# Kernel optimization log

Measured on AMD Instinct MI355X. Metric: run time of the kernel, lower is better.

Reference implementation:

```python
import jax, jax.numpy as jnp
import numpy as np
import math

B, N, M = 128, 32, 64           # batch, num_agents, num_other
OBS, ACT = 128, 16              # obs_input_dim, num_actions
D_QK = 128                      # obs_output_dim (== obs_output_dim_other)
D_AV = 64                       # obs_act_output_dim (== other)
F_IN = OBS + ACT                # obs_act_input_dim = 144


def _xavier(key, shape):
    fan_in, fan_out = shape[0], shape[1]
    limit = math.sqrt(6.0 / (fan_in + fan_out))
    return jax.random.uniform(key, shape, jnp.float32, -limit, limit)


def setup_inputs() -> dict:
    key = jax.random.key(0)
    ks = jax.random.split(key, 13)
    return {
        "states": jax.random.normal(ks[0], (B, N, OBS), jnp.float32),
        "policies": jax.random.uniform(ks[1], (B, N, ACT), jnp.float32),
        "actions": jax.random.uniform(ks[2], (B, N, ACT), jnp.float32),
        "states_other": jax.random.normal(ks[3], (B, M, OBS), jnp.float32),
        "actions_other": jax.random.uniform(ks[4], (B, M, ACT), jnp.float32),
        # weights stored as [in, out] (x @ W == nn.Linear without bias)
        "W_key": _xavier(ks[5], (OBS, D_QK)),
        "W_query": _xavier(ks[6], (OBS, D_QK)),
        "W_av": _xavier(ks[7], (F_IN, D_AV)),
        "W_key_other": _xavier(ks[8], (OBS, D_QK)),
        "W_query_other": _xavier(ks[9], (OBS, D_QK)),
        "W_av_other": _xavier(ks[10], (F_IN, D_AV)),
        "W_f1": _xavier(ks[11], (2 * D_AV, 64)),
        "W_f2": _xavier(ks[12], (64, 1)),
    }


def reference(states, policies, actions, states_other, actions_other,
              W_key, W_query, W_av, W_key_other, W_query_other,
              W_av_other, W_f1, W_f2):
    b, n, _ = states.shape
    obs_actions = jnp.concatenate([states, actions], axis=-1)   # [B,N,F_IN]
    obs_policy = jnp.concatenate([states, policies], axis=-1)   # [B,N,F_IN]

    key_obs = states @ W_key                                    # [B,N,D_QK]
    query_obs = states @ W_query                                # [B,N,D_QK]
    d_k = W_key.shape[1]
    weight = jax.nn.softmax(
        jnp.einsum('bid,bjd->bij', query_obs, key_obs) / math.sqrt(d_k), axis=-1)
    ret_weight = weight

    # place_policies is identity on (j,k): oap[b,j,k] = obs_policy[b,k] if j==k else obs_actions[b,k]
    eye = jnp.eye(n, dtype=states.dtype)[None, :, :, None]       # [1,N,N,1]
    oap = eye * obs_policy[:, None, :, :] + (1.0 - eye) * obs_actions[:, None, :, :]
    attention_values = jnp.tanh(oap @ W_av)                      # [B,N,N,D_AV] (j,k)

    # repeat-mul-sum == weighted reduction over k: wav[b,i,j,d] = sum_k w[b,i,k] av[b,j,k,d]
    wav = jnp.einsum('bik,bjkd->bijd', weight, attention_values)  # [B,N,N,D_AV]

    obs_actions_other = jnp.concatenate([states_other, actions_other], axis=-1)
    keys_other = states_other @ W_key_other                      # [B,M,D_QK]
    query_agent = states @ W_query_other                         # [B,N,D_QK]
    av_other = jnp.tanh(obs_actions_other @ W_av_other)          # [B,M,D_AV]
    d_k_o = W_key_other.shape[1]
    weight_other = jax.nn.softmax(
        jnp.einsum('bid,bmd->bim', query_agent, keys_other) / math.sqrt(d_k_o), axis=-1)
    wav_other = jnp.einsum('bim,bmd->bid', weight_other, av_other)  # [B,N,D_AV]

    # broadcast the per-agent other-branch features across the j axis for the concat
    wav_other_b = jnp.broadcast_to(wav_other[:, :, None, :], wav.shape[:-1] + (wav_other.shape[-1],))
    node_features = jnp.concatenate([wav, wav_other_b], axis=-1)  # [B,N,N,2*D_AV]

    h = jax.nn.leaky_relu(node_features @ W_f1, negative_slope=0.01)
    value = h @ W_f2                                              # [B,N,N,1]
    return value, ret_weight, weight_other
```

## Files before the change

kernel.cpp:

```cpp
#include <hip/hip_runtime.h>
#include <math.h>

#define WS_WQK   0
#define WS_WQKO  16384
#define WS_AVA   32768
#define WS_AVO   294912
#define WS_DPROJ 819200

#define INV_SQRT_DK 0.08838834764831845f

__device__ __forceinline__ float dot4(float4 a, float4 b) {
  return a.x*b.x + a.y*b.y + a.z*b.z + a.w*b.w;
}
__device__ __forceinline__ void fma4(float4& a, const float4 w, const float s) {
  a.x += w.x*s; a.y += w.y*s; a.z += w.z*s; a.w += w.w*s;
}

__global__ __launch_bounds__(256) void k1_pre(
    const float* __restrict__ g_states, const float* __restrict__ g_pol,
    const float* __restrict__ g_act, const float* __restrict__ g_so,
    const float* __restrict__ g_ao,
    const float* __restrict__ Wq, const float* __restrict__ Wk,
    const float* __restrict__ Wqo, const float* __restrict__ Wko,
    const float* __restrict__ W_av, const float* __restrict__ W_avo,
    const float* __restrict__ W_f1, float* __restrict__ ws)
{
  __shared__ __align__(16) float pool[8448];
  const int t = threadIdx.x;
  int blk = blockIdx.x;

  if (blk < 32) {
    const float* A; const float* Bm; float* O;
    if (blk < 16) { A = Wq;  Bm = Wk;  O = ws + WS_WQK; }
    else          { A = Wqo; Bm = Wko; O = ws + WS_WQKO; blk -= 16; }
    const int tr = (blk >> 2) << 5;
    const int tc = (blk & 3) << 5;
    float* sA = pool;
    float* sB = pool + 4224;
    const float4* a4 = (const float4*)(A + tr * 128);
    const float4* b4 = (const float4*)(Bm + tc * 128);
    #pragma unroll
    for (int u = 0; u < 4; ++u) {
      int f = t + u * 256;
      int r = f >> 5, c4 = f & 31;
      *(float4*)(sA + r*132 + c4*4) = a4[f];
      *(float4*)(sB + r*132 + c4*4) = b4[f];
    }
    __syncthreads();
    const int e = t & 31, cl0 = t >> 5;
    float acc[4] = {0,0,0,0};
    #pragma unroll 4
    for (int d4 = 0; d4 < 32; ++d4) {
      float4 bv = *(const float4*)(sB + e*132 + d4*4);
      #pragma unroll
      for (int rr = 0; rr < 4; ++rr) {
        float4 av = *(const float4*)(sA + (cl0 + rr*8)*132 + d4*4);
        acc[rr] += dot4(av, bv);
      }
    }
    #pragma unroll
    for (int rr = 0; rr < 4; ++rr)
      O[(tr + cl0 + rr*8)*128 + tc + e] = acc[rr];
    return;
  }
  blk -= 32;

  if (blk < 128) {
    const int b = blk;
    float* s_pre = pool;
    float* s_dl  = pool + 4224;
    {
      const int wv_  = t >> 6;
      const int ap   = wv_ & 1;
      const int rh   = wv_ >> 1;
      const int lane = t & 63;
      const float* gs = g_states + b*4096 + rh*16*128;
      const float* gt = (ap ? g_pol : g_act) + b*512 + rh*16*16;
      float acc[16];
      #pragma unroll
      for (int r = 0; r < 16; ++r) acc[r] = 0.f;
      #pragma unroll 4
      for (int c4 = 0; c4 < 32; ++c4) {
        const float w0 = W_av[(c4*4+0)*64 + lane];
        const float w1 = W_av[(c4*4+1)*64 + lane];
        const float w2 = W_av[(c4*4+2)*64 + lane];
        const float w3 = W_av[(c4*4+3)*64 + lane];
        #pragma unroll
        for (int r = 0; r < 16; ++r) {
          float4 sv = *(const float4*)(gs + r*128 + c4*4);
          acc[r] += sv.x*w0 + sv.y*w1 + sv.z*w2 + sv.w*w3;
        }
      }
      #pragma unroll
      for (int c4 = 0; c4 < 4; ++c4) {
        const float w0 = W_av[(128 + c4*4+0)*64 + lane];
        const float w1 = W_av[(128 + c4*4+1)*64 + lane];
        const float w2 = W_av[(128 + c4*4+2)*64 + lane];
        const float w3 = W_av[(128 + c4*4+3)*64 + lane];
        #pragma unroll
        for (int r = 0; r < 16; ++r) {
          float4 sv = *(const float4*)(gt + r*16 + c4*4);
          acc[r] += sv.x*w0 + sv.y*w1 + sv.z*w2 + sv.w*w3;
        }
      }
      #pragma unroll
      for (int r = 0; r < 16; ++r)
        s_pre[(rh*16 + r)*132 + ap*64 + lane] = acc[r];
    }
    __syncthreads();
    {
      const int r = t >> 3, d0 = (t & 7) << 3;
      float4 a0 = *(const float4*)(s_pre + r*132 + d0);
      float4 a1 = *(const float4*)(s_pre + r*132 + d0 + 4);
      float4 p0 = *(const float4*)(s_pre + r*132 + 64 + d0);
      float4 p1 = *(const float4*)(s_pre + r*132 + 64 + d0 + 4);
      float4 va0, va1, dl0, dl1;
      va0.x = tanhf(a0.x); va0.y = tanhf(a0.y); va0.z = tanhf(a0.z); va0.w = tanhf(a0.w);
      va1.x = tanhf(a1.x); va1.y = tanhf(a1.y); va1.z = tanhf(a1.z); va1.w = tanhf(a1.w);
      dl0.x = tanhf(p0.x) - va0.x; dl0.y = tanhf(p0.y) - va0.y;
      dl0.z = tanhf(p0.z) - va0.z; dl0.w = tanhf(p0.w) - va0.w;
      dl1.x = tanhf(p1.x) - va1.x; dl1.y = tanhf(p1.y) - va1.y;
      dl1.z = tanhf(p1.z) - va1.z; dl1.w = tanhf(p1.w) - va1.w;
      *(float4*)(ws + WS_AVA + b*2048 + r*64 + d0)     = va0;
      *(float4*)(ws + WS_AVA + b*2048 + r*64 + d0 + 4) = va1;
      *(float4*)(s_dl + r*68 + d0)     = dl0;
      *(float4*)(s_dl + r*68 + d0 + 4) = dl1;
    }
    __syncthreads();
    {
      const int h = t & 63;
      const int j0 = (t >> 6) << 3;
      float acc[8] = {0,0,0,0,0,0,0,0};
      #pragma unroll 4
      for (int d4 = 0; d4 < 16; ++d4) {
        float w0 = W_f1[(d4*4+0)*64 + h];
        float w1 = W_f1[(d4*4+1)*64 + h];
        float w2 = W_f1[(d4*4+2)*64 + h];
        float w3 = W_f1[(d4*4+3)*64 + h];
        #pragma unroll
        for (int q = 0; q < 8; ++q) {
          float4 dv = *(const float4*)(s_dl + (j0+q)*68 + d4*4);
          acc[q] += dv.x*w0 + dv.y*w1 + dv.z*w2 + dv.w*w3;
        }
      }
      #pragma unroll
      for (int q = 0; q < 8; ++q)
        ws[WS_DPROJ + b*2048 + (j0+q)*64 + h] = acc[q];
    }
    return;
  }
  blk -= 128;

  {
    const int b = blk >> 1, m0 = (blk & 1) << 5;
    const int wv_  = t >> 6;
    const int lane = t & 63;
    const float* gso = g_so + (b*64 + m0 + wv_*8) * 128;
    const float* gao = g_ao + (b*64 + m0 + wv_*8) * 16;
    float acc[8];
    #pragma unroll
    for (int r = 0; r < 8; ++r) acc[r] = 0.f;
    #pragma unroll 4
    for (int c4 = 0; c4 < 32; ++c4) {
      const float w0 = W_avo[(c4*4+0)*64 + lane];
      const float w1 = W_avo[(c4*4+1)*64 + lane];
      const float w2 = W_avo[(c4*4+2)*64 + lane];
      const float w3 = W_avo[(c4*4+3)*64 + lane];
      #pragma unroll
      for (int r = 0; r < 8; ++r) {
        float4 sv = *(const float4*)(gso + r*128 + c4*4);
        acc[r] += sv.x*w0 + sv.y*w1 + sv.z*w2 + sv.w*w3;
      }
    }
    #pragma unroll
    for (int c4 = 0; c4 < 4; ++c4) {
      const float w0 = W_avo[(128 + c4*4+0)*64 + lane];
      const float w1 = W_avo[(128 + c4*4+1)*64 + lane];
      const float w2 = W_avo[(128 + c4*4+2)*64 + lane];
      const float w3 = W_avo[(128 + c4*4+3)*64 + lane];
      #pragma unroll
      for (int r = 0; r < 8; ++r) {
        float4 sv = *(const float4*)(gao + r*16 + c4*4);
        acc[r] += sv.x*w0 + sv.y*w1 + sv.z*w2 + sv.w*w3;
      }
    }
    #pragma unroll
    for (int r = 0; r < 8; ++r)
      ws[WS_AVO + b*4096 + (m0 + wv_*8 + r)*64 + lane] = tanhf(acc[r]);
  }
}

__global__ __launch_bounds__(256) void k2_main(
    const float* __restrict__ g_states, const float* __restrict__ g_so,
    const float* __restrict__ W_f1, const float* __restrict__ W_f2,
    const float* __restrict__ ws, float* __restrict__ out)
{
  __shared__ __align__(16) float pool[17472];
  float* s_st   = pool;
  float* s_red  = pool + 4352;
  float* s_avA  = pool + 4352;
  float* s_dp   = pool + 6528;
  float* s_avO  = pool;
  float* s_P    = pool + 12800;
  float* s_w    = pool + 14944;
  float* s_wo   = pool + 15232;
  float* s_S    = pool + 15776;
  float* s_wavo = pool + 16320;
  float* s_base = pool + 16864;
  float* s_wf2  = pool + 17408;

  const int t = threadIdx.x;
  const int b = blockIdx.x >> 2;
  const int i0 = (blockIdx.x & 3) << 3;

  {
    const float4* gs4 = (const float4*)(g_states + b * 4096);
    #pragma unroll
    for (int u = 0; u < 4; ++u) {
      int f = t + u * 256;
      int r = f >> 5, c4 = f & 31;
      *(float4*)(s_st + r*132 + c4*4) = gs4[f];
    }
    if (t < 16) *(float4*)(s_wf2 + t*4) = ((const float4*)W_f2)[t];
  }

  {
    const int wave = t >> 6;
    const int col  = t & 63;
    const float* Wp = (col < 32) ? (ws + WS_WQK + col*4)
                                 : (ws + WS_WQKO + (col-32)*4);
    const float* srow = g_states + b*4096 + i0*128 + wave*32;
    float4 acc[8];
    #pragma unroll
    for (int r = 0; r < 8; ++r) acc[r] = make_float4(0.f,0.f,0.f,0.f);
    #pragma unroll 2
    for (int c4 = 0; c4 < 8; ++c4) {
      float4 sv[8];
      #pragma unroll
      for (int r = 0; r < 8; ++r)
        sv[r] = *(const float4*)(srow + r*128 + c4*4);
      #pragma unroll
      for (int k = 0; k < 4; ++k) {
        float4 wv = *(const float4*)(Wp + (wave*32 + c4*4 + k)*128);
        #pragma unroll
        for (int r = 0; r < 8; ++r)
          fma4(acc[r], wv, ((const float*)&sv[r])[k]);
      }
    }
    #pragma unroll
    for (int r = 0; r < 8; ++r)
      *(float4*)(s_red + ((wave*8 + r)*66 + col)*4) = acc[r];
  }
  __syncthreads();
  {
    const int r = t >> 5, cp = t & 31;
    #pragma unroll
    for (int s2 = 0; s2 < 2; ++s2) {
      const int col = cp*2 + s2;
      float4 a0 = *(const float4*)(s_red + ((0*8 + r)*66 + col)*4);
      float4 a1 = *(const float4*)(s_red + ((1*8 + r)*66 + col)*4);
      float4 a2 = *(const float4*)(s_red + ((2*8 + r)*66 + col)*4);
      float4 a3 = *(const float4*)(s_red + ((3*8 + r)*66 + col)*4);
      float4 s4;
      s4.x = (a0.x + a1.x) + (a2.x + a3.x);
      s4.y = (a0.y + a1.y) + (a2.y + a3.y);
      s4.z = (a0.z + a1.z) + (a2.z + a3.z);
      s4.w = (a0.w + a1.w) + (a2.w + a3.w);
      *(float4*)(s_P + r*268 + col*4) = s4;
    }
  }
  __syncthreads();

  {
    const int r = t >> 5, j = t & 31;
    float acc = 0.f;
    #pragma unroll 8
    for (int e4 = 0; e4 < 32; ++e4) {
      float4 p4  = *(const float4*)(s_P + r*268 + e4*4);
      float4 st4 = *(const float4*)(s_st + j*132 + e4*4);
      acc += dot4(p4, st4);
    }
    acc *= INV_SQRT_DK;
    float mx = acc;
    for (int off = 16; off; off >>= 1) mx = fmaxf(mx, __shfl_xor(mx, off, 32));
    float ev = __expf(acc - mx);
    float sum = ev;
    for (int off = 16; off; off >>= 1) sum += __shfl_xor(sum, off, 32);
    float wn = ev / sum;
    out[131072 + b*1024 + (i0 + r)*32 + j] = wn;
    s_w[r*36 + j] = wn;
  }
  __syncthreads();

  for (int tt = 0; tt < 2; ++tt) {
    const float4* gt4 = (const float4*)(g_so + (b*64 + tt*32) * 128);
    #pragma unroll
    for (int u = 0; u < 4; ++u) {
      int f = t + u * 256;
      int r = f >> 5, c4 = f & 31;
      *(float4*)(s_st + r*132 + c4*4) = gt4[f];
    }
    __syncthreads();
    const int r = t >> 5, m = t & 31;
    float acc = 0.f;
    #pragma unroll 8
    for (int c4 = 0; c4 < 32; ++c4) {
      float4 p4  = *(const float4*)(s_P + r*268 + 128 + c4*4);
      float4 st4 = *(const float4*)(s_st + m*132 + c4*4);
      acc += dot4(p4, st4);
    }
    s_wo[r*68 + tt*32 + m] = acc * INV_SQRT_DK;
    __syncthreads();
  }

  #pragma unroll
  for (int p = 0; p < 2; ++p) {
    const int r = (t >> 6) + (p << 2), l = t & 63;
    float v = s_wo[r*68 + l];
    float mx = v;
    for (int off = 32; off; off >>= 1) mx = fmaxf(mx, __shfl_xor(mx, off, 64));
    float ev = __expf(v - mx);
    float sum = ev;
    for (int off = 32; off; off >>= 1) sum += __shfl_xor(sum, off, 64);
    float wn = ev / sum;
    out[262144 + b*2048 + (i0 + r)*64 + l] = wn;
    s_wo[r*68 + l] = wn;
  }
  #pragma unroll
  for (int u = 0; u < 2; ++u) {
    int f = t + u * 256;
    int k = f >> 4, dq = f & 15;
    *(float4*)(s_avA + k*68 + dq*4) = ((const float4*)(ws + WS_AVA + b*2048))[f];
    *(float4*)(s_dp  + k*68 + dq*4) = ((const float4*)(ws + WS_DPROJ + b*2048))[f];
  }
  #pragma unroll
  for (int u = 0; u < 4; ++u) {
    int f = t + u * 256;
    int m = f >> 4, dq = f & 15;
    *(float4*)(s_avO + m*68 + dq*4) = ((const float4*)(ws + WS_AVO + b*4096))[f];
  }
  __syncthreads();

  if (t < 128) {
    const int i = t >> 4, dq = (t & 15) << 2;
    float4 acc = {0,0,0,0};
    #pragma unroll 4
    for (int k = 0; k < 32; ++k) {
      float4 a4 = *(const float4*)(s_avA + k*68 + dq);
      float wv = s_w[i*36 + k];
      acc.x += wv*a4.x; acc.y += wv*a4.y; acc.z += wv*a4.z; acc.w += wv*a4.w;
    }
    *(float4*)(s_S + i*68 + dq) = acc;
  } else {
    const int tt2 = t - 128;
    const int i = tt2 >> 4, dq = (tt2 & 15) << 2;
    float4 acc = {0,0,0,0};
    #pragma unroll 4
    for (int m = 0; m < 64; ++m) {
      float4 a4 = *(const float4*)(s_avO + m*68 + dq);
      float wv = s_wo[i*68 + m];
      acc.x += wv*a4.x; acc.y += wv*a4.y; acc.z += wv*a4.z; acc.w += wv*a4.w;
    }
    *(float4*)(s_wavo + i*68 + dq) = acc;
  }
  __syncthreads();

  {
    const int h = t & 63, g = (t >> 6) << 1;
    float a0 = 0.f, a1 = 0.f;
    #pragma unroll 4
    for (int d = 0; d < 64; ++d) {
      float w1v = W_f1[d*64 + h];
      float w2v = W_f1[(64 + d)*64 + h];
      a0 += s_S[g*68 + d]*w1v + s_wavo[g*68 + d]*w2v;
      a1 += s_S[(g+1)*68 + d]*w1v + s_wavo[(g+1)*68 + d]*w2v;
    }
    s_base[g*68 + h] = a0;
    s_base[(g+1)*68 + h] = a1;
  }
  __syncthreads();

  {
    const int i = t >> 5, j = t & 31;
    const float wij = s_w[i*36 + j];
    float acc = 0.f;
    #pragma unroll 4
    for (int hq = 0; hq < 16; ++hq) {
      float4 b4 = *(const float4*)(s_base + i*68 + hq*4);
      float4 d4 = *(const float4*)(s_dp + j*68 + hq*4);
      float4 f4 = *(const float4*)(s_wf2 + hq*4);
      float p0 = b4.x + wij*d4.x; p0 = p0 > 0.f ? p0 : 0.01f*p0;
      float p1 = b4.y + wij*d4.y; p1 = p1 > 0.f ? p1 : 0.01f*p1;
      float p2 = b4.z + wij*d4.z; p2 = p2 > 0.f ? p2 : 0.01f*p2;
      float p3 = b4.w + wij*d4.w; p3 = p3 > 0.f ? p3 : 0.01f*p3;
      acc += p0*f4.x + p1*f4.y + p2*f4.z + p3*f4.w;
    }
    out[b*1024 + (i0 + i)*32 + j] = acc;
  }
}

extern "C" void kernel_launch(void* const* d_in, const int* in_sizes, int n_in,
                              void* d_out, int out_size, void* d_ws, size_t ws_size,
                              hipStream_t stream) {
  const float* states        = (const float*)d_in[0];
  const float* policies      = (const float*)d_in[1];
  const float* actions       = (const float*)d_in[2];
  const float* states_other  = (const float*)d_in[3];
  const float* actions_other = (const float*)d_in[4];
  const float* W_key         = (const float*)d_in[5];
  const float* W_query       = (const float*)d_in[6];
  const float* W_av          = (const float*)d_in[7];
  const float* W_key_other   = (const float*)d_in[8];
  const float* W_query_other = (const float*)d_in[9];
  const float* W_av_other    = (const float*)d_in[10];
  const float* W_f1          = (const float*)d_in[11];
  const float* W_f2          = (const float*)d_in[12];
  float* out = (float*)d_out;
  float* ws  = (float*)d_ws;

  k1_pre<<<416, 256, 0, stream>>>(states, policies, actions, states_other,
                                  actions_other, W_query, W_key,
                                  W_query_other, W_key_other, W_av, W_av_other,
                                  W_f1, ws);
  k2_main<<<512, 256, 0, stream>>>(states, states_other, W_f1, W_f2, ws, out);
}
```

Measured before the change: 129.6 us.

## Split k1 work across more blocks and double k2 threads per block

k1 now splits each batch's agent-value and delta-projection work into two half-row blocks and the other-agent branch into quarter blocks, giving 800 blocks instead of 416. k2 moves to 512 threads per block. Its dot-product and reduction loops are split in halves and combined with cross-half shuffles or a second partial buffer. The aim is more parallelism and latency hiding on a small, launch-bound workload, at the cost of extra shuffles, redundant weight loads and higher register pressure under the new launch bounds.

```diff
diff --git a/kernel.cpp b/kernel.cpp
--- a/kernel.cpp
+++ b/kernel.cpp
@@ -16,7 +16,7 @@
   a.x += w.x*s; a.y += w.y*s; a.z += w.z*s; a.w += w.w*s;
 }
 
-__global__ __launch_bounds__(256) void k1_pre(
+__global__ __launch_bounds__(256, 4) void k1_pre(
     const float* __restrict__ g_states, const float* __restrict__ g_pol,
     const float* __restrict__ g_act, const float* __restrict__ g_so,
     const float* __restrict__ g_ao,
@@ -65,20 +65,21 @@
   }
   blk -= 32;
 
-  if (blk < 128) {
-    const int b = blk;
+  if (blk < 256) {
+    const int b  = blk >> 1;
+    const int jh = blk & 1;
     float* s_pre = pool;
-    float* s_dl  = pool + 4224;
+    float* s_dl  = pool + 2112;
     {
       const int wv_  = t >> 6;
       const int ap   = wv_ & 1;
-      const int rh   = wv_ >> 1;
+      const int rq   = wv_ >> 1;
       const int lane = t & 63;
-      const float* gs = g_states + b*4096 + rh*16*128;
-      const float* gt = (ap ? g_pol : g_act) + b*512 + rh*16*16;
-      float acc[16];
-      #pragma unroll
-      for (int r = 0; r < 16; ++r) acc[r] = 0.f;
+      const float* gs = g_states + b*4096 + (jh*16 + rq*8)*128;
+      const float* gt = (ap ? g_pol : g_act) + b*512 + (jh*16 + rq*8)*16;
+      float acc[8];
+      #pragma unroll
+      for (int r = 0; r < 8; ++r) acc[r] = 0.f;
       #pragma unroll 4
       for (int c4 = 0; c4 < 32; ++c4) {
         const float w0 = W_av[(c4*4+0)*64 + lane];
@@ -86,7 +87,7 @@
         const float w2 = W_av[(c4*4+2)*64 + lane];
         const float w3 = W_av[(c4*4+3)*64 + lane];
         #pragma unroll
-        for (int r = 0; r < 16; ++r) {
+        for (int r = 0; r < 8; ++r) {
           float4 sv = *(const float4*)(gs + r*128 + c4*4);
           acc[r] += sv.x*w0 + sv.y*w1 + sv.z*w2 + sv.w*w3;
         }
@@ -98,39 +99,32 @@
         const float w2 = W_av[(128 + c4*4+2)*64 + lane];
         const float w3 = W_av[(128 + c4*4+3)*64 + lane];
         #pragma unroll
-        for (int r = 0; r < 16; ++r) {
+        for (int r = 0; r < 8; ++r) {
           float4 sv = *(const float4*)(gt + r*16 + c4*4);
           acc[r] += sv.x*w0 + sv.y*w1 + sv.z*w2 + sv.w*w3;
         }
       }
       #pragma unroll
-      for (int r = 0; r < 16; ++r)
-        s_pre[(rh*16 + r)*132 + ap*64 + lane] = acc[r];
+      for (int r = 0; r < 8; ++r)
+        s_pre[(rq*8 + r)*132 + ap*64 + lane] = acc[r];
     }
     __syncthreads();
     {
-      const int r = t >> 3, d0 = (t & 7) << 3;
+      const int r = t >> 4, d0 = (t & 15) << 2;
       float4 a0 = *(const float4*)(s_pre + r*132 + d0);
-      float4 a1 = *(const float4*)(s_pre + r*132 + d0 + 4);
       float4 p0 = *(const float4*)(s_pre + r*132 + 64 + d0);
-      float4 p1 = *(const float4*)(s_pre + r*132 + 64 + d0 + 4);
-      float4 va0, va1, dl0, dl1;
+      float4 va0, dl0;
       va0.x = tanhf(a0.x); va0.y = tanhf(a0.y); va0.z = tanhf(a0.z); va0.w = tanhf(a0.w);
-      va1.x = tanhf(a1.x); va1.y = tanhf(a1.y); va1.z = tanhf(a1.z); va1.w = tanhf(a1.w);
       dl0.x = tanhf(p0.x) - va0.x; dl0.y = tanhf(p0.y) - va0.y;
       dl0.z = tanhf(p0.z) - va0.z; dl0.w = tanhf(p0.w) - va0.w;
-      dl1.x = tanhf(p1.x) - va1.x; dl1.y = tanhf(p1.y) - va1.y;
-      dl1.z = tanhf(p1.z) - va1.z; dl1.w = tanhf(p1.w) - va1.w;
-      *(float4*)(ws + WS_AVA + b*2048 + r*64 + d0)     = va0;
-      *(float4*)(ws + WS_AVA + b*2048 + r*64 + d0 + 4) = va1;
-      *(float4*)(s_dl + r*68 + d0)     = dl0;
-      *(float4*)(s_dl + r*68 + d0 + 4) = dl1;
+      *(float4*)(ws + WS_AVA + b*2048 + (jh*16 + r)*64 + d0) = va0;
+      *(float4*)(s_dl + r*68 + d0) = dl0;
     }
     __syncthreads();
     {
       const int h = t & 63;
-      const int j0 = (t >> 6) << 3;
-      float acc[8] = {0,0,0,0,0,0,0,0};
+      const int j0 = (t >> 6) << 2;
+      float acc[4] = {0,0,0,0};
       #pragma unroll 4
       for (int d4 = 0; d4 < 16; ++d4) {
         float w0 = W_f1[(d4*4+0)*64 + h];
@@ -138,28 +132,26 @@
         float w2 = W_f1[(d4*4+2)*64 + h];
         float w3 = W_f1[(d4*4+3)*64 + h];
         #pragma unroll
-        for (int q = 0; q < 8; ++q) {
+        for (int q = 0; q < 4; ++q) {
           float4 dv = *(const float4*)(s_dl + (j0+q)*68 + d4*4);
           acc[q] += dv.x*w0 + dv.y*w1 + dv.z*w2 + dv.w*w3;
         }
       }
       #pragma unroll
-      for (int q = 0; q < 8; ++q)
-        ws[WS_DPROJ + b*2048 + (j0+q)*64 + h] = acc[q];
+      for (int q = 0; q < 4; ++q)
+        ws[WS_DPROJ + b*2048 + (jh*16 + j0+q)*64 + h] = acc[q];
     }
     return;
   }
-  blk -= 128;
-
-  {
-    const int b = blk >> 1, m0 = (blk & 1) << 5;
+  blk -= 256;
+
+  {
+    const int b = blk >> 2, m0 = (blk & 3) << 4;
     const int wv_  = t >> 6;
     const int lane = t & 63;
-    const float* gso = g_so + (b*64 + m0 + wv_*8) * 128;
-    const float* gao = g_ao + (b*64 + m0 + wv_*8) * 16;
-    float acc[8];
-    #pragma unroll
-    for (int r = 0; r < 8; ++r) acc[r] = 0.f;
+    const float* gso = g_so + (b*64 + m0 + wv_*4) * 128;
+    const float* gao = g_ao + (b*64 + m0 + wv_*4) * 16;
+    float acc[4] = {0.f, 0.f, 0.f, 0.f};
     #pragma unroll 4
     for (int c4 = 0; c4 < 32; ++c4) {
       const float w0 = W_avo[(c4*4+0)*64 + lane];
@@ -167,7 +159,7 @@
       const float w2 = W_avo[(c4*4+2)*64 + lane];
       const float w3 = W_avo[(c4*4+3)*64 + lane];
       #pragma unroll
-      for (int r = 0; r < 8; ++r) {
+      for (int r = 0; r < 4; ++r) {
         float4 sv = *(const float4*)(gso + r*128 + c4*4);
         acc[r] += sv.x*w0 + sv.y*w1 + sv.z*w2 + sv.w*w3;
       }
@@ -179,18 +171,18 @@
       const float w2 = W_avo[(128 + c4*4+2)*64 + lane];
       const float w3 = W_avo[(128 + c4*4+3)*64 + lane];
       #pragma unroll
-      for (int r = 0; r < 8; ++r) {
+      for (int r = 0; r < 4; ++r) {
         float4 sv = *(const float4*)(gao + r*16 + c4*4);
         acc[r] += sv.x*w0 + sv.y*w1 + sv.z*w2 + sv.w*w3;
       }
     }
     #pragma unroll
-    for (int r = 0; r < 8; ++r)
-      ws[WS_AVO + b*4096 + (m0 + wv_*8 + r)*64 + lane] = tanhf(acc[r]);
+    for (int r = 0; r < 4; ++r)
+      ws[WS_AVO + b*4096 + (m0 + wv_*4 + r)*64 + lane] = tanhf(acc[r]);
   }
 }
 
-__global__ __launch_bounds__(256) void k2_main(
+__global__ __launch_bounds__(512, 4) void k2_main(
     const float* __restrict__ g_states, const float* __restrict__ g_so,
     const float* __restrict__ W_f1, const float* __restrict__ W_f2,
     const float* __restrict__ ws, float* __restrict__ out)
@@ -216,8 +208,8 @@
   {
     const float4* gs4 = (const float4*)(g_states + b * 4096);
     #pragma unroll
-    for (int u = 0; u < 4; ++u) {
-      int f = t + u * 256;
+    for (int u = 0; u < 2; ++u) {
+      int f = t + u * 512;
       int r = f >> 5, c4 = f & 31;
       *(float4*)(s_st + r*132 + c4*4) = gs4[f];
     }
@@ -226,60 +218,60 @@
 
   {
     const int wave = t >> 6;
+    const int kc   = wave & 3;
+    const int rh   = wave >> 2;
     const int col  = t & 63;
     const float* Wp = (col < 32) ? (ws + WS_WQK + col*4)
                                  : (ws + WS_WQKO + (col-32)*4);
-    const float* srow = g_states + b*4096 + i0*128 + wave*32;
-    float4 acc[8];
-    #pragma unroll
-    for (int r = 0; r < 8; ++r) acc[r] = make_float4(0.f,0.f,0.f,0.f);
+    const float* srow = g_states + b*4096 + (i0 + rh*4)*128 + kc*32;
+    float4 acc[4];
+    #pragma unroll
+    for (int r = 0; r < 4; ++r) acc[r] = make_float4(0.f,0.f,0.f,0.f);
     #pragma unroll 2
     for (int c4 = 0; c4 < 8; ++c4) {
-      float4 sv[8];
-      #pragma unroll
-      for (int r = 0; r < 8; ++r)
+      float4 sv[4];
+      #pragma unroll
+      for (int r = 0; r < 4; ++r)
         sv[r] = *(const float4*)(srow + r*128 + c4*4);
       #pragma unroll
       for (int k = 0; k < 4; ++k) {
-        float4 wv = *(const float4*)(Wp + (wave*32 + c4*4 + k)*128);
+        float4 wv = *(const float4*)(Wp + (kc*32 + c4*4 + k)*128);
         #pragma unroll
-        for (int r = 0; r < 8; ++r)
+        for (int r = 0; r < 4; ++r)
           fma4(acc[r], wv, ((const float*)&sv[r])[k]);
       }
     }
     #pragma unroll
-    for (int r = 0; r < 8; ++r)
-      *(float4*)(s_red + ((wave*8 + r)*66 + col)*4) = acc[r];
-  }
-  __syncthreads();
-  {
-    const int r = t >> 5, cp = t & 31;
-    #pragma unroll
-    for (int s2 = 0; s2 < 2; ++s2) {
-      const int col = cp*2 + s2;
-      float4 a0 = *(const float4*)(s_red + ((0*8 + r)*66 + col)*4);
-      float4 a1 = *(const float4*)(s_red + ((1*8 + r)*66 + col)*4);
-      float4 a2 = *(const float4*)(s_red + ((2*8 + r)*66 + col)*4);
-      float4 a3 = *(const float4*)(s_red + ((3*8 + r)*66 + col)*4);
-      float4 s4;
-      s4.x = (a0.x + a1.x) + (a2.x + a3.x);
-      s4.y = (a0.y + a1.y) + (a2.y + a3.y);
-      s4.z = (a0.z + a1.z) + (a2.z + a3.z);
-      s4.w = (a0.w + a1.w) + (a2.w + a3.w);
-      *(float4*)(s_P + r*268 + col*4) = s4;
-    }
-  }
-  __syncthreads();
-
-  {
-    const int r = t >> 5, j = t & 31;
+    for (int r = 0; r < 4; ++r)
+      *(float4*)(s_red + ((kc*8 + rh*4 + r)*66 + col)*4) = acc[r];
+  }
+  __syncthreads();
+  {
+    const int r = t >> 6, col = t & 63;
+    float4 a0 = *(const float4*)(s_red + ((0*8 + r)*66 + col)*4);
+    float4 a1 = *(const float4*)(s_red + ((1*8 + r)*66 + col)*4);
+    float4 a2 = *(const float4*)(s_red + ((2*8 + r)*66 + col)*4);
+    float4 a3 = *(const float4*)(s_red + ((3*8 + r)*66 + col)*4);
+    float4 s4;
+    s4.x = (a0.x + a1.x) + (a2.x + a3.x);
+    s4.y = (a0.y + a1.y) + (a2.y + a3.y);
+    s4.z = (a0.z + a1.z) + (a2.z + a3.z);
+    s4.w = (a0.w + a1.w) + (a2.w + a3.w);
+    *(float4*)(s_P + r*268 + col*4) = s4;
+  }
+  __syncthreads();
+
+  {
+    const int r = t >> 6, j = t & 31, half = (t >> 5) & 1;
+    const int e0 = half << 4;
     float acc = 0.f;
     #pragma unroll 8
-    for (int e4 = 0; e4 < 32; ++e4) {
-      float4 p4  = *(const float4*)(s_P + r*268 + e4*4);
-      float4 st4 = *(const float4*)(s_st + j*132 + e4*4);
+    for (int e4 = 0; e4 < 16; ++e4) {
+      float4 p4  = *(const float4*)(s_P + r*268 + (e0 + e4)*4);
+      float4 st4 = *(const float4*)(s_st + j*132 + (e0 + e4)*4);
       acc += dot4(p4, st4);
     }
+    acc += __shfl_xor(acc, 32, 64);
     acc *= INV_SQRT_DK;
     float mx = acc;
     for (int off = 16; off; off >>= 1) mx = fmaxf(mx, __shfl_xor(mx, off, 32));
@@ -287,35 +279,38 @@
     float sum = ev;
     for (int off = 16; off; off >>= 1) sum += __shfl_xor(sum, off, 32);
     float wn = ev / sum;
-    out[131072 + b*1024 + (i0 + r)*32 + j] = wn;
-    s_w[r*36 + j] = wn;
+    if (half == 0) {
+      out[131072 + b*1024 + (i0 + r)*32 + j] = wn;
+      s_w[r*36 + j] = wn;
+    }
   }
   __syncthreads();
 
   for (int tt = 0; tt < 2; ++tt) {
     const float4* gt4 = (const float4*)(g_so + (b*64 + tt*32) * 128);
     #pragma unroll
-    for (int u = 0; u < 4; ++u) {
-      int f = t + u * 256;
+    for (int u = 0; u < 2; ++u) {
+      int f = t + u * 512;
       int r = f >> 5, c4 = f & 31;
       *(float4*)(s_st + r*132 + c4*4) = gt4[f];
     }
     __syncthreads();
-    const int r = t >> 5, m = t & 31;
+    const int r = t >> 6, m = t & 31, half = (t >> 5) & 1;
+    const int c0 = half << 4;
     float acc = 0.f;
     #pragma unroll 8
-    for (int c4 = 0; c4 < 32; ++c4) {
-      float4 p4  = *(const float4*)(s_P + r*268 + 128 + c4*4);
-      float4 st4 = *(const float4*)(s_st + m*132 + c4*4);
+    for (int c4 = 0; c4 < 16; ++c4) {
+      float4 p4  = *(const float4*)(s_P + r*268 + 128 + (c0 + c4)*4);
+      float4 st4 = *(const float4*)(s_st + m*132 + (c0 + c4)*4);
       acc += dot4(p4, st4);
     }
-    s_wo[r*68 + tt*32 + m] = acc * INV_SQRT_DK;
+    acc += __shfl_xor(acc, 32, 64);
+    if (half == 0) s_wo[r*68 + tt*32 + m] = acc * INV_SQRT_DK;
     __syncthreads();
   }
 
-  #pragma unroll
-  for (int p = 0; p < 2; ++p) {
-    const int r = (t >> 6) + (p << 2), l = t & 63;
+  {
+    const int r = t >> 6, l = t & 63;
     float v = s_wo[r*68 + l];
     float mx = v;
     for (int off = 32; off; off >>= 1) mx = fmaxf(mx, __shfl_xor(mx, off, 64));
@@ -326,16 +321,15 @@
     out[262144 + b*2048 + (i0 + r)*64 + l] = wn;
     s_wo[r*68 + l] = wn;
   }
-  #pragma unroll
-  for (int u = 0; u < 2; ++u) {
-    int f = t + u * 256;
+  {
+    int f = t;
     int k = f >> 4, dq = f & 15;
     *(float4*)(s_avA + k*68 + dq*4) = ((const float4*)(ws + WS_AVA + b*2048))[f];
     *(float4*)(s_dp  + k*68 + dq*4) = ((const float4*)(ws + WS_DPROJ + b*2048))[f];
   }
   #pragma unroll
-  for (int u = 0; u < 4; ++u) {
-    int f = t + u * 256;
+  for (int u = 0; u < 2; ++u) {
+    int f = t + u * 512;
     int m = f >> 4, dq = f & 15;
     *(float4*)(s_avO + m*68 + dq*4) = ((const float4*)(ws + WS_AVO + b*4096))[f];
   }
@@ -351,41 +345,42 @@
       acc.x += wv*a4.x; acc.y += wv*a4.y; acc.z += wv*a4.z; acc.w += wv*a4.w;
     }
     *(float4*)(s_S + i*68 + dq) = acc;
-  } else {
+  } else if (t < 384) {
     const int tt2 = t - 128;
-    const int i = tt2 >> 4, dq = (tt2 & 15) << 2;
+    const int mh = tt2 >> 7;
+    const int i = (tt2 & 127) >> 4, dq = (tt2 & 15) << 2;
     float4 acc = {0,0,0,0};
     #pragma unroll 4
-    for (int m = 0; m < 64; ++m) {
+    for (int mm = 0; mm < 32; ++mm) {
+      const int m = mh*32 + mm;
       float4 a4 = *(const float4*)(s_avO + m*68 + dq);
       float wv = s_wo[i*68 + m];
       acc.x += wv*a4.x; acc.y += wv*a4.y; acc.z += wv*a4.z; acc.w += wv*a4.w;
     }
-    *(float4*)(s_wavo + i*68 + dq) = acc;
-  }
-  __syncthreads();
-
-  {
-    const int h = t & 63, g = (t >> 6) << 1;
-    float a0 = 0.f, a1 = 0.f;
+    float* dst = mh ? (s_P + i*68 + dq) : (s_wavo + i*68 + dq);
+    *(float4*)dst = acc;
+  }
+  __syncthreads();
+
+  {
+    const int h = t & 63, i = t >> 6;
+    float a0 = 0.f;
     #pragma unroll 4
     for (int d = 0; d < 64; ++d) {
       float w1v = W_f1[d*64 + h];
       float w2v = W_f1[(64 + d)*64 + h];
-      a0 += s_S[g*68 + d]*w1v + s_wavo[g*68 + d]*w2v;
-      a1 += s_S[(g+1)*68 + d]*w1v + s_wavo[(g+1)*68 + d]*w2v;
-    }
-    s_base[g*68 + h] = a0;
-    s_base[(g+1)*68 + h] = a1;
-  }
-  __syncthreads();
-
-  {
-    const int i = t >> 5, j = t & 31;
+      a0 += s_S[i*68 + d]*w1v + (s_wavo[i*68 + d] + s_P[i*68 + d])*w2v;
+    }
+    s_base[i*68 + h] = a0;
+  }
+  __syncthreads();
+
+  {
+    const int i = t >> 6, j = t & 31, half = (t >> 5) & 1;
     const float wij = s_w[i*36 + j];
     float acc = 0.f;
     #pragma unroll 4
-    for (int hq = 0; hq < 16; ++hq) {
+    for (int hq = half*8; hq < half*8 + 8; ++hq) {
       float4 b4 = *(const float4*)(s_base + i*68 + hq*4);
       float4 d4 = *(const float4*)(s_dp + j*68 + hq*4);
       float4 f4 = *(const float4*)(s_wf2 + hq*4);
@@ -395,7 +390,9 @@
       float p3 = b4.w + wij*d4.w; p3 = p3 > 0.f ? p3 : 0.01f*p3;
       acc += p0*f4.x + p1*f4.y + p2*f4.z + p3*f4.w;
     }
-    out[b*1024 + (i0 + i)*32 + j] = acc;
+    acc += __shfl_xor(acc, 32, 64);
+    if (half == 0)
+      out[b*1024 + (i0 + i)*32 + j] = acc;
   }
 }
 
@@ -418,9 +415,9 @@
   float* out = (float*)d_out;
   float* ws  = (float*)d_ws;
 
-  k1_pre<<<416, 256, 0, stream>>>(states, policies, actions, states_other,
+  k1_pre<<<800, 256, 0, stream>>>(states, policies, actions, states_other,
                                   actions_other, W_query, W_key,
                                   W_query_other, W_key_other, W_av, W_av_other,
                                   W_f1, ws);
-  k2_main<<<512, 256, 0, stream>>>(states, states_other, W_f1, W_f2, ws, out);
+  k2_main<<<512, 512, 0, stream>>>(states, states_other, W_f1, W_f2, ws, out);
 }
```

After: 138.6 us. 1.07x slower.
